# Kernel optimization log

Measured on AMD Instinct MI355X. Metric: run time of the kernel, lower is better.

## Reference

```python
import jax, jax.numpy as jnp
import numpy as np

KERNEL_SIZE = 257

def conv1d_same_padding(x, weights):
    # x: [B,1,L], weights: [K]  (cross-correlation, matching torch F.conv1d)
    K = weights.shape[0]
    pad_total = K - 1
    if pad_total % 2 != 0:
        x = jnp.pad(x, ((0, 0), (0, 0), (0, 1)))
    p = pad_total // 2
    w = weights.reshape(1, 1, K)  # [out_ch, in_ch, K]
    return jax.lax.conv_general_dilated(
        x, w, window_strides=(1,), padding=[(p, p)],
        dimension_numbers=('NCW', 'OIW', 'NCW'))

def topk_absolutes_1d(x, k):
    # keep top-k |values| per sample, zero the rest (scatter semantics of repo)
    B = x.shape[0]
    xf = x.reshape(B, -1)
    _, idx = jax.lax.top_k(jnp.abs(xf), k)            # [B, k]
    vals = jnp.take_along_axis(xf, idx, axis=-1)      # [B, k]
    out = jnp.zeros_like(xf).at[jnp.arange(B)[:, None], idx].set(vals)
    return out.reshape(x.shape)

def setup_inputs() -> dict:
    key = jax.random.key(0)
    k1, k2 = jax.random.split(key)
    x = jax.random.normal(k1, (64, 1, 262144), dtype=jnp.float32)
    weights = jax.random.normal(k2, (KERNEL_SIZE,), dtype=jnp.float32) * 0.1
    return {"x": x, "weights": weights, "k": 2048}

def reference(x, weights, k):
    similarity = conv1d_same_padding(x, weights)
    extrema = topk_absolutes_1d(similarity, k)
    reconstruction = conv1d_same_padding(extrema, weights)
    return (reconstruction, similarity, extrema)
```

## Files before the change

### kernel.cpp

```cpp
#include <hip/hip_runtime.h>

#define L_LEN 262144
#define KSZ 257
#define BLK 256
#define TILE 4096
#define HALO (KSZ - 1)
#define LDSA (TILE + HALO)
#define NBIN 4096
#define SEGCAP 256
#define NCHUNK 32
#define CANDMAX 6144
#define TIECAP 1024
#define WCAP 2048

#define LDSW 4368
#define LDSP 4416
#define NJ 9

typedef __attribute__((ext_vector_type(8))) short bf16x8;
typedef __attribute__((ext_vector_type(4))) float f32x4;

__device__ __forceinline__ ushort bf16_rne(float f) {
    const unsigned u = __float_as_uint(f);
    return (ushort)((u + 0x7FFFu + ((u >> 16) & 1u)) >> 16);
}

__device__ __forceinline__ int swz8(int G) { return G ^ ((G >> 3) & 7); }

__global__ __launch_bounds__(BLK) void zero_ws_kernel(uint4* __restrict__ p, int n16) {
    const int i = blockIdx.x * BLK + threadIdx.x;
    if (i < n16) p[i] = make_uint4(0u, 0u, 0u, 0u);
}

template<bool HIST>
__global__ __launch_bounds__(BLK) void mfma_conv_kernel(const float* __restrict__ in,
                                                        const float* __restrict__ w,
                                                        float* __restrict__ out,
                                                        unsigned* __restrict__ ghist) {
    __shared__ ushort xh[LDSP];
    __shared__ ushort xl[LDSP];
    __shared__ unsigned shist[HIST ? NBIN : 1];

    const int t = threadIdx.x;
    const int sample = blockIdx.x >> 6;
    const int tile   = blockIdx.x & 63;
    const float* xrow = in  + (size_t)sample * L_LEN;
    float*       orow = out + (size_t)sample * L_LEN;
    const int tstart = tile * TILE;
    const int gbase  = tstart - (KSZ / 2);

    if (HIST) for (int h = t; h < NBIN; h += BLK) shist[h] = 0u;

    for (int i4 = t; i4 < LDSW / 4; i4 += BLK) {
        const int g = gbase + i4 * 4;
        float4 v;
        if ((unsigned)g <= (unsigned)(L_LEN - 4)) v = *(const float4*)(xrow + g);
        else v = make_float4(0.f, 0.f, 0.f, 0.f);
        const float vv[4] = {v.x, v.y, v.z, v.w};
        ushort h4[4], l4[4];
#pragma unroll
        for (int e = 0; e < 4; ++e) {
            const ushort h = bf16_rne(vv[e]);
            h4[e] = h;
            l4[e] = bf16_rne(vv[e] - __uint_as_float((unsigned)h << 16));
        }
        const int off = (swz8(i4 >> 1) << 3) + ((i4 & 1) << 2);
        *(ushort4*)(&xh[off]) = make_ushort4(h4[0], h4[1], h4[2], h4[3]);
        *(ushort4*)(&xl[off]) = make_ushort4(l4[0], l4[1], l4[2], l4[3]);
    }

    const int lane = t & 63;
    const int cc = lane & 15;
    const int bb = lane >> 4;
    bf16x8 Bh[NJ], Bl[NJ];
#pragma unroll
    for (int f = 0; f < NJ; ++f) {
#pragma unroll
        for (int e = 0; e < 8; ++e) {
            const int j = f * 32 + 8 * bb + e - cc;
            const float v = ((unsigned)j <= 256u) ? w[j] : 0.f;
            const ushort h = bf16_rne(v);
            Bh[f][e] = (short)h;
            Bl[f][e] = (short)bf16_rne(v - __uint_as_float((unsigned)h << 16));
        }
    }
    __syncthreads();

    const int wv = t >> 6;
    const int wvbase = wv * 1024;
    const int arow = 16 * cc + 8 * bb;

    f32x4 acc[4] = {};
#pragma unroll
    for (int f = 0; f < NJ; ++f) {
#pragma unroll
        for (int st = 0; st < 4; ++st) {
            const int ao = wvbase + st * 256 + f * 32 + arow;
            const int po = swz8(ao >> 3) << 3;
            const bf16x8 Ah = *(const bf16x8*)(&xh[po]);
            const bf16x8 Al = *(const bf16x8*)(&xl[po]);
            acc[st] = __builtin_amdgcn_mfma_f32_16x16x32_bf16(Ah, Bh[f], acc[st], 0, 0, 0);
            acc[st] = __builtin_amdgcn_mfma_f32_16x16x32_bf16(Ah, Bl[f], acc[st], 0, 0, 0);
            acc[st] = __builtin_amdgcn_mfma_f32_16x16x32_bf16(Al, Bh[f], acc[st], 0, 0, 0);
        }
    }

#pragma unroll
    for (int st = 0; st < 4; ++st) {
        const int mbase = tstart + wvbase + st * 256 + 64 * bb + cc;
#pragma unroll
        for (int r = 0; r < 4; ++r) {
            const float v = acc[st][r];
            orow[mbase + 16 * r] = v;
            if (HIST) {
                const unsigned u = (__float_as_uint(v) & 0x7fffffffu) >> 19;
                atomicAdd(&shist[u], 1u);
            }
        }
    }

    if (HIST) {
        __syncthreads();
        for (int h = t; h < NBIN; h += BLK) {
            const unsigned c = shist[h];
            if (c) atomicAdd(&ghist[(size_t)sample * NBIN + h], c);
        }
    }
}

__global__ __launch_bounds__(1024) void bin_select_kernel(const unsigned* __restrict__ ghist,
                                                          int2* __restrict__ sel,
                                                          const int* __restrict__ kptr) {
    __shared__ int ss[1024];
    const int t = threadIdx.x;
    const int b = blockIdx.x;
    const unsigned* hist = ghist + (size_t)b * NBIN;
    const int k = kptr[0];

    const int g4 = t * 4;
    const int h0 = (int)hist[g4], h1 = (int)hist[g4 + 1],
              h2 = (int)hist[g4 + 2], h3 = (int)hist[g4 + 3];
    ss[t] = h0 + h1 + h2 + h3;
    __syncthreads();
    for (int off = 1; off < 1024; off <<= 1) {
        const int add = (t + off < 1024) ? ss[t + off] : 0;
        __syncthreads();
        ss[t] += add;
        __syncthreads();
    }
    const int S0 = ss[t];
    const int S4 = (t < 1023) ? ss[t + 1] : 0;
    const int S1 = S0 - h0, S2 = S1 - h1, S3 = S2 - h2;
    if (S0 >= k && S1 < k) sel[b] = make_int2(g4,     k - S1);
    if (S1 >= k && S2 < k) sel[b] = make_int2(g4 + 1, k - S2);
    if (S2 >= k && S3 < k) sel[b] = make_int2(g4 + 2, k - S3);
    if (S3 >= k && S4 < k) sel[b] = make_int2(g4 + 3, k - S4);
}

__global__ __launch_bounds__(BLK) void refine_kernel(const float* __restrict__ in,
                                                     const float* __restrict__ w,
                                                     float* __restrict__ sim,
                                                     const int2* __restrict__ sel,
                                                     int* __restrict__ delta) {
    __shared__ float lx[LDSA + LDSA / 16];
    __shared__ float lw[KSZ];
    __shared__ int   wl[WCAP];
    __shared__ int   s_cnt, s_delta;
    const int t = threadIdx.x;
    const int sample = blockIdx.x >> 6;
    const int tile   = blockIdx.x & 63;
    const float* xrow = in  + (size_t)sample * L_LEN;
    float*       srow = sim + (size_t)sample * L_LEN;
    const int tstart = tile * TILE;
    const int gbase  = tstart - (KSZ / 2);
    const unsigned selBin = (unsigned)sel[sample].x;

    if (t == 0) { s_cnt = 0; s_delta = 0; }
    for (int i = t; i < KSZ; i += BLK) lw[i] = w[i];
    for (int i4 = t; i4 < LDSA / 4; i4 += BLK) {
        const int g = gbase + i4 * 4;
        float4 v;
        if ((unsigned)g <= (unsigned)(L_LEN - 4)) v = *(const float4*)(xrow + g);
        else v = make_float4(0.f, 0.f, 0.f, 0.f);
        const int ib = i4 * 4;
        const int p = ib + (ib >> 4);
        lx[p] = v.x; lx[p + 1] = v.y; lx[p + 2] = v.z; lx[p + 3] = v.w;
    }
    __syncthreads();

#pragma unroll
    for (int q = 0; q < 4; ++q) {
        const int m0 = t * 16 + q * 4;
        const float4 sv = *(const float4*)(srow + tstart + m0);
        const float vv[4] = {sv.x, sv.y, sv.z, sv.w};
#pragma unroll
        for (int e = 0; e < 4; ++e) {
            const unsigned u12 = (__float_as_uint(vv[e]) & 0x7fffffffu) >> 19;
            if ((unsigned)(u12 + 1u - selBin) <= 2u) {
                const int p = atomicAdd(&s_cnt, 1);
                if (p < WCAP) wl[p] = (m0 + e) | ((int)(u12 > selBin) << 30);
            }
        }
    }
    __syncthreads();

    int cnt = s_cnt; if (cnt > WCAP) cnt = WCAP;
    for (int p = t; p < cnt; p += BLK) {
        const int rec = wl[p];
        const int ml = rec & 0x3FFFFFFF;
        const int pre_gt = (rec >> 30) & 1;
        float acc = 0.f;
        for (int j = 0; j < KSZ; ++j) {
            const int el = ml + j;
            acc = fmaf(lw[j], lx[el + (el >> 4)], acc);
        }
        const unsigned pu = (__float_as_uint(acc) & 0x7fffffffu) >> 19;
        const int post_gt = (pu > selBin) ? 1 : 0;
        if (pre_gt != post_gt) atomicAdd(&s_delta, post_gt - pre_gt);
        srow[tstart + ml] = acc;
    }
    __syncthreads();
    if (t == 0 && s_delta != 0) atomicAdd(&delta[sample], s_delta);
}

__global__ __launch_bounds__(BLK) void write_gather_kernel(const float* __restrict__ sim,
                                                           float* __restrict__ ext,
                                                           uint2* __restrict__ cand,
                                                           int* __restrict__ segCnt,
                                                           const int2* __restrict__ sel) {
    __shared__ int s_cnt;
    const int t = threadIdx.x;
    const int b = blockIdx.x >> 5;
    const int chunk = blockIdx.x & (NCHUNK - 1);
    const unsigned selBin = (unsigned)sel[b].x;
    const float* row  = sim + (size_t)b * L_LEN;
    float*       erow = ext + (size_t)b * L_LEN;
    uint2* seg = cand + ((size_t)b * NCHUNK + chunk) * SEGCAP;
    const int base = chunk * (L_LEN / NCHUNK);

    if (t == 0) s_cnt = 0;
    __syncthreads();

    for (int i = t; i < (L_LEN / NCHUNK) / 4; i += BLK) {
        const int g = base + i * 4;
        const float4 v = *(const float4*)(row + g);
        const float vv[4] = {v.x, v.y, v.z, v.w};
        float o[4];
#pragma unroll
        for (int e = 0; e < 4; ++e) {
            const unsigned u = __float_as_uint(vv[e]) & 0x7fffffffu;
            const unsigned u12 = u >> 19;
            o[e] = (u12 > selBin) ? vv[e] : 0.f;
            if ((unsigned)(selBin - u12) <= 1u) {
                const int p = atomicAdd(&s_cnt, 1);
                if (p < SEGCAP) seg[p] = make_uint2(u, (unsigned)(g + e));
            }
        }
        *(float4*)(erow + g) = make_float4(o[0], o[1], o[2], o[3]);
    }
    __syncthreads();
    if (t == 0) segCnt[b * NCHUNK + chunk] = (s_cnt < SEGCAP) ? s_cnt : SEGCAP;
}

__global__ __launch_bounds__(1024) void finalize_kernel(const float* __restrict__ sim,
                                                        float* __restrict__ ext,
                                                        const uint2* __restrict__ cand,
                                                        const int* __restrict__ segCnt,
                                                        const int2* __restrict__ sel,
                                                        const int* __restrict__ delta) {
    __shared__ int hist[1024];
    __shared__ int ss[1024];
    __shared__ uint2 list[CANDMAX];
    __shared__ int tie[TIECAP];
    __shared__ int scnt[NCHUNK];
    __shared__ int segoff[NCHUNK + 1];
    __shared__ int s_b1, s_kk2, s_Tlow, s_m, s_tieCnt;
    const int t = threadIdx.x;
    const int b = blockIdx.x;
    const float* srow = sim + (size_t)b * L_LEN;
    float*       erow = ext + (size_t)b * L_LEN;
    const unsigned selBin = (unsigned)sel[b].x;
    const unsigned vbase = (selBin > 0 ? selBin - 1 : 0) << 19;
    int kk = sel[b].y - delta[b];

    if (t < NCHUNK) scnt[t] = segCnt[b * NCHUNK + t];
    __syncthreads();
    if (t == 0) {
        int a = 0;
        for (int s = 0; s < NCHUNK; ++s) { segoff[s] = a; a += scnt[s]; }
        segoff[NCHUNK] = a;
    }
    if (t == 1) s_tieCnt = 0;
    __syncthreads();
    int cnt = segoff[NCHUNK]; if (cnt > CANDMAX) cnt = CANDMAX;
    if (kk <= 0) return;
    if (kk > cnt) kk = cnt;

    for (int j = t; j < NCHUNK * SEGCAP; j += 1024) {
        const int s = j >> 8;
        const int i = j & (SEGCAP - 1);
        if (i < scnt[s]) {
            const int dst = segoff[s] + i;
            if (dst < CANDMAX)
                list[dst] = cand[((size_t)b * NCHUNK + s) * SEGCAP + i];
        }
    }
    __syncthreads();

    hist[t] = 0;
    __syncthreads();
    for (int p = t; p < cnt; p += 1024)
        atomicAdd(&hist[(list[p].x - vbase) >> 10], 1);
    __syncthreads();
    ss[t] = hist[t];
    __syncthreads();
    for (int off = 1; off < 1024; off <<= 1) {
        const int add = (t + off < 1024) ? ss[t + off] : 0;
        __syncthreads();
        ss[t] += add;
        __syncthreads();
    }
    {
        const int S = ss[t];
        const int Sn = (t < 1023) ? ss[t + 1] : 0;
        if (S >= kk && Sn < kk) { s_b1 = t; s_kk2 = kk - Sn; }
    }
    __syncthreads();
    const int b1 = s_b1, kk2 = s_kk2;

    hist[t] = 0;
    __syncthreads();
    for (int p = t; p < cnt; p += 1024) {
        const unsigned v = list[p].x - vbase;
        if ((int)(v >> 10) == b1) atomicAdd(&hist[v & 1023u], 1);
    }
    __syncthreads();
    ss[t] = hist[t];
    __syncthreads();
    for (int off = 1; off < 1024; off <<= 1) {
        const int add = (t + off < 1024) ? ss[t + off] : 0;
        __syncthreads();
        ss[t] += add;
        __syncthreads();
    }
    {
        const int S = ss[t];
        const int Sn = (t < 1023) ? ss[t + 1] : 0;
        if (S >= kk2 && Sn < kk2) { s_Tlow = (b1 << 10) | t; s_m = kk2 - Sn; }
    }
    __syncthreads();
    const unsigned Tlow = (unsigned)s_Tlow;
    const int m = s_m;

    for (int p = t; p < cnt; p += 1024) {
        const unsigned v = list[p].x - vbase;
        const int idx = (int)list[p].y;
        if (v > Tlow) erow[idx] = srow[idx];
        else if (v == Tlow) {
            const int q = atomicAdd(&s_tieCnt, 1);
            if (q < TIECAP) tie[q] = idx;
        }
    }
    __syncthreads();
    int tc = s_tieCnt; if (tc > TIECAP) tc = TIECAP;
    for (int p = t; p < tc; p += 1024) {
        const int idx = tie[p];
        int rank = 0;
        for (int q = 0; q < tc; ++q) rank += (tie[q] < idx) ? 1 : 0;
        if (rank < m) erow[idx] = srow[idx];
    }
}

extern "C" void kernel_launch(void* const* d_in, const int* in_sizes, int n_in,
                              void* d_out, int out_size, void* d_ws, size_t ws_size,
                              hipStream_t stream) {
    const float* x    = (const float*)d_in[0];
    const float* w    = (const float*)d_in[1];
    const int*   kptr = (const int*)d_in[2];
    float* out = (float*)d_out;

    const int total = in_sizes[0];
    const int B = total / L_LEN;

    float* recon = out;
    float* sim   = out + (size_t)total;
    float* ext   = out + 2 * (size_t)total;

    uint8_t* ws = (uint8_t*)d_ws;
    unsigned* ghist  = (unsigned*)ws;
    int*      delta  = (int*)(ws + 1048576);
    int2*     sel    = (int2*)(ws + 1048576 + 1024);
    int*      segCnt = (int*)(ws + 1048576 + 2048);
    uint2*    cand   = (uint2*)(ws + 1048576 + 2048 + 8192);

    const int n16 = (1048576 + 1024) / 16;
    zero_ws_kernel<<<dim3((n16 + BLK - 1) / BLK), BLK, 0, stream>>>((uint4*)ws, n16);

    mfma_conv_kernel<true><<<dim3(B * 64), BLK, 0, stream>>>(x, w, sim, ghist);
    bin_select_kernel<<<dim3(B), 1024, 0, stream>>>(ghist, sel, kptr);
    refine_kernel<<<dim3(B * 64), BLK, 0, stream>>>(x, w, sim, sel, delta);
    write_gather_kernel<<<dim3(B * NCHUNK), BLK, 0, stream>>>(sim, ext, cand, segCnt, sel);
    finalize_kernel<<<dim3(B), 1024, 0, stream>>>(sim, ext, cand, segCnt, sel, delta);
    mfma_conv_kernel<false><<<dim3(B * 64), BLK, 0, stream>>>(ext, w, recon, nullptr);
}
```

Measured before the change: 192.0 us.

## Fuse fp32 refinement of borderline elements into the write/gather pass

Removes the separate refine kernel. Its exact fp32 recomputation of near-threshold convolution outputs now happens inside write_gather. The fused kernel lists borderline elements per chunk into a larger LDS worklist and recomputes them by reading x directly from global memory. It writes their extrema value, records candidates and accumulates the count delta, which saves one launch and one full pass over the similarity buffer. In exchange, the per-element recompute uses uncoalesced global loads instead of an LDS tile. The refined values are also no longer written back into the similarity output, which may change what that output contains.

```diff
diff --git a/kernel.cpp b/kernel.cpp
--- a/kernel.cpp
+++ b/kernel.cpp
@@ -4,14 +4,13 @@
 #define KSZ 257
 #define BLK 256
 #define TILE 4096
-#define HALO (KSZ - 1)
-#define LDSA (TILE + HALO)
 #define NBIN 4096
 #define SEGCAP 256
 #define NCHUNK 32
+#define CHUNK (L_LEN / NCHUNK)
 #define CANDMAX 6144
 #define TIECAP 1024
-#define WCAP 2048
+#define WGCAP CHUNK
 
 #define LDSW 4368
 #define LDSP 4416
@@ -157,91 +156,32 @@
     if (S3 >= k && S4 < k) sel[b] = make_int2(g4 + 3, k - S4);
 }
 
-__global__ __launch_bounds__(BLK) void refine_kernel(const float* __restrict__ in,
-                                                     const float* __restrict__ w,
-                                                     float* __restrict__ sim,
-                                                     const int2* __restrict__ sel,
-                                                     int* __restrict__ delta) {
-    __shared__ float lx[LDSA + LDSA / 16];
-    __shared__ float lw[KSZ];
-    __shared__ int   wl[WCAP];
-    __shared__ int   s_cnt, s_delta;
-    const int t = threadIdx.x;
-    const int sample = blockIdx.x >> 6;
-    const int tile   = blockIdx.x & 63;
-    const float* xrow = in  + (size_t)sample * L_LEN;
-    float*       srow = sim + (size_t)sample * L_LEN;
-    const int tstart = tile * TILE;
-    const int gbase  = tstart - (KSZ / 2);
-    const unsigned selBin = (unsigned)sel[sample].x;
-
-    if (t == 0) { s_cnt = 0; s_delta = 0; }
-    for (int i = t; i < KSZ; i += BLK) lw[i] = w[i];
-    for (int i4 = t; i4 < LDSA / 4; i4 += BLK) {
-        const int g = gbase + i4 * 4;
-        float4 v;
-        if ((unsigned)g <= (unsigned)(L_LEN - 4)) v = *(const float4*)(xrow + g);
-        else v = make_float4(0.f, 0.f, 0.f, 0.f);
-        const int ib = i4 * 4;
-        const int p = ib + (ib >> 4);
-        lx[p] = v.x; lx[p + 1] = v.y; lx[p + 2] = v.z; lx[p + 3] = v.w;
-    }
-    __syncthreads();
-
-#pragma unroll
-    for (int q = 0; q < 4; ++q) {
-        const int m0 = t * 16 + q * 4;
-        const float4 sv = *(const float4*)(srow + tstart + m0);
-        const float vv[4] = {sv.x, sv.y, sv.z, sv.w};
-#pragma unroll
-        for (int e = 0; e < 4; ++e) {
-            const unsigned u12 = (__float_as_uint(vv[e]) & 0x7fffffffu) >> 19;
-            if ((unsigned)(u12 + 1u - selBin) <= 2u) {
-                const int p = atomicAdd(&s_cnt, 1);
-                if (p < WCAP) wl[p] = (m0 + e) | ((int)(u12 > selBin) << 30);
-            }
-        }
-    }
-    __syncthreads();
-
-    int cnt = s_cnt; if (cnt > WCAP) cnt = WCAP;
-    for (int p = t; p < cnt; p += BLK) {
-        const int rec = wl[p];
-        const int ml = rec & 0x3FFFFFFF;
-        const int pre_gt = (rec >> 30) & 1;
-        float acc = 0.f;
-        for (int j = 0; j < KSZ; ++j) {
-            const int el = ml + j;
-            acc = fmaf(lw[j], lx[el + (el >> 4)], acc);
-        }
-        const unsigned pu = (__float_as_uint(acc) & 0x7fffffffu) >> 19;
-        const int post_gt = (pu > selBin) ? 1 : 0;
-        if (pre_gt != post_gt) atomicAdd(&s_delta, post_gt - pre_gt);
-        srow[tstart + ml] = acc;
-    }
-    __syncthreads();
-    if (t == 0 && s_delta != 0) atomicAdd(&delta[sample], s_delta);
-}
-
-__global__ __launch_bounds__(BLK) void write_gather_kernel(const float* __restrict__ sim,
+__global__ __launch_bounds__(BLK) void write_gather_kernel(const float* __restrict__ x,
+                                                           const float* __restrict__ w,
+                                                           const float* __restrict__ sim,
                                                            float* __restrict__ ext,
                                                            uint2* __restrict__ cand,
                                                            int* __restrict__ segCnt,
-                                                           const int2* __restrict__ sel) {
-    __shared__ int s_cnt;
+                                                           const int2* __restrict__ sel,
+                                                           int* __restrict__ delta) {
+    __shared__ int wl[WGCAP];
+    __shared__ float lw[KSZ];
+    __shared__ int s_cnt, s_wcnt, s_delta;
     const int t = threadIdx.x;
     const int b = blockIdx.x >> 5;
     const int chunk = blockIdx.x & (NCHUNK - 1);
     const unsigned selBin = (unsigned)sel[b].x;
+    const float* xrow = x   + (size_t)b * L_LEN;
     const float* row  = sim + (size_t)b * L_LEN;
     float*       erow = ext + (size_t)b * L_LEN;
     uint2* seg = cand + ((size_t)b * NCHUNK + chunk) * SEGCAP;
-    const int base = chunk * (L_LEN / NCHUNK);
-
-    if (t == 0) s_cnt = 0;
-    __syncthreads();
-
-    for (int i = t; i < (L_LEN / NCHUNK) / 4; i += BLK) {
+    const int base = chunk * CHUNK;
+
+    if (t == 0) { s_cnt = 0; s_wcnt = 0; s_delta = 0; }
+    for (int i = t; i < KSZ; i += BLK) lw[i] = w[i];
+    __syncthreads();
+
+    for (int i = t; i < CHUNK / 4; i += BLK) {
         const int g = base + i * 4;
         const float4 v = *(const float4*)(row + g);
         const float vv[4] = {v.x, v.y, v.z, v.w};
@@ -250,16 +190,45 @@
         for (int e = 0; e < 4; ++e) {
             const unsigned u = __float_as_uint(vv[e]) & 0x7fffffffu;
             const unsigned u12 = u >> 19;
-            o[e] = (u12 > selBin) ? vv[e] : 0.f;
-            if ((unsigned)(selBin - u12) <= 1u) {
-                const int p = atomicAdd(&s_cnt, 1);
-                if (p < SEGCAP) seg[p] = make_uint2(u, (unsigned)(g + e));
+            if ((unsigned)(u12 + 1u - selBin) <= 2u) {
+                o[e] = 0.f;
+                const int p = atomicAdd(&s_wcnt, 1);
+                wl[p] = (g + e) | ((int)(u12 > selBin) << 30);
+            } else {
+                o[e] = (u12 > selBin) ? vv[e] : 0.f;
             }
         }
         *(float4*)(erow + g) = make_float4(o[0], o[1], o[2], o[3]);
     }
     __syncthreads();
-    if (t == 0) segCnt[b * NCHUNK + chunk] = (s_cnt < SEGCAP) ? s_cnt : SEGCAP;
+
+    const int wc = s_wcnt;
+    for (int p = t; p < wc; p += BLK) {
+        const int rec = wl[p];
+        const int gidx = rec & 0x3FFFFFFF;
+        const int pre_gt = (rec >> 30) & 1;
+        const int gb = gidx - (KSZ / 2);
+        float acc = 0.f;
+        for (int j = 0; j < KSZ; ++j) {
+            const int gx = gb + j;
+            const float xv = ((unsigned)gx < (unsigned)L_LEN) ? xrow[gx] : 0.f;
+            acc = fmaf(lw[j], xv, acc);
+        }
+        const unsigned u = __float_as_uint(acc) & 0x7fffffffu;
+        const unsigned u12 = u >> 19;
+        const int post_gt = (u12 > selBin) ? 1 : 0;
+        if (post_gt != pre_gt) atomicAdd(&s_delta, post_gt - pre_gt);
+        if (post_gt) erow[gidx] = acc;
+        if ((unsigned)(selBin - u12) <= 1u) {
+            const int p2 = atomicAdd(&s_cnt, 1);
+            if (p2 < SEGCAP) seg[p2] = make_uint2(u, (unsigned)gidx);
+        }
+    }
+    __syncthreads();
+    if (t == 0) {
+        segCnt[b * NCHUNK + chunk] = (s_cnt < SEGCAP) ? s_cnt : SEGCAP;
+        if (s_delta != 0) atomicAdd(&delta[b], s_delta);
+    }
 }
 
 __global__ __launch_bounds__(1024) void finalize_kernel(const float* __restrict__ sim,
@@ -398,8 +367,7 @@
 
     mfma_conv_kernel<true><<<dim3(B * 64), BLK, 0, stream>>>(x, w, sim, ghist);
     bin_select_kernel<<<dim3(B), 1024, 0, stream>>>(ghist, sel, kptr);
-    refine_kernel<<<dim3(B * 64), BLK, 0, stream>>>(x, w, sim, sel, delta);
-    write_gather_kernel<<<dim3(B * NCHUNK), BLK, 0, stream>>>(sim, ext, cand, segCnt, sel);
+    write_gather_kernel<<<dim3(B * NCHUNK), BLK, 0, stream>>>(x, w, sim, ext, cand, segCnt, sel, delta);
     finalize_kernel<<<dim3(B), 1024, 0, stream>>>(sim, ext, cand, segCnt, sel, delta);
     mfma_conv_kernel<false><<<dim3(B * 64), BLK, 0, stream>>>(ext, w, recon, nullptr);
 }
```

After: 222.1 us. +15.7%, slower.
